# Performance work log

Measured on AMD Instinct MI355X. Metric: run time of the kernel, lower is better.

## Reference

```python
import jax, jax.numpy as jnp
import numpy as np

TIMESTEPS = 1000

def _cosine_schedule(T, s=0.008):
    # Nichol & Dhariwal cosine schedule
    x = np.linspace(0.0, T, T + 1, dtype=np.float64)
    acp = np.cos(((x / T) + s) / (1.0 + s) * np.pi / 2.0) ** 2
    acp = acp / acp[0]
    betas = np.clip(1.0 - acp[1:] / acp[:-1], 1e-4, 0.999)
    alphas_cumprod = np.cumprod(1.0 - betas)
    return (betas.astype(np.float32),
            np.sqrt(alphas_cumprod).astype(np.float32),
            np.sqrt(1.0 - alphas_cumprod).astype(np.float32))

BETAS, SQRT_ACP, SQRT_OM_ACP = _cosine_schedule(TIMESTEPS)

B = 2048            # crystals
N_PER = 64          # atoms per crystal (uniform ragged groups)
N = B * N_PER       # total atoms
NODE_DIM = 64
N_SPECIES = 100

def setup_inputs() -> dict:
    key = jax.random.key(0)
    ks = jax.random.split(key, 10)
    frac_coords = jax.random.uniform(ks[0], (N, 3), dtype=jnp.float32)
    noise = jax.random.normal(ks[1], (N, 3), dtype=jnp.float32)
    pred_noise = jax.random.normal(ks[2], (N, 3), dtype=jnp.float32)
    h_final = jax.random.normal(ks[3], (N, NODE_DIM), dtype=jnp.float32)
    # lattice: identity-dominated cells ~5 Angstrom with small perturbation
    lattice = 5.0 * jnp.eye(3, dtype=jnp.float32)[None] + 0.2 * jax.random.normal(ks[4], (B, 3, 3), dtype=jnp.float32)
    W1 = jax.random.normal(ks[5], (NODE_DIM, 128), dtype=jnp.float32) * (1.0 / np.sqrt(NODE_DIM))
    b1 = jnp.zeros((128,), dtype=jnp.float32)
    W2 = jax.random.normal(ks[6], (128, N_SPECIES), dtype=jnp.float32) * (1.0 / np.sqrt(128.0))
    b2 = jnp.zeros((N_SPECIES,), dtype=jnp.float32)
    t = jax.random.randint(ks[7], (B,), 0, TIMESTEPS)
    batch_indices = jnp.repeat(jnp.arange(B), N_PER)
    species = jax.random.randint(ks[8], (N,), 0, N_SPECIES)
    return {"frac_coords": frac_coords, "noise": noise, "pred_noise": pred_noise,
            "h_final": h_final, "lattice": lattice, "W1": W1, "b1": b1,
            "W2": W2, "b2": b2, "t": t, "batch_indices": batch_indices,
            "species": species}

def reference(frac_coords, noise, pred_noise, h_final, lattice, W1, b1, W2, b2,
              t, batch_indices, species):
    sqrt_acp = jnp.asarray(SQRT_ACP)
    sqrt_om = jnp.asarray(SQRT_OM_ACP)
    t_nodes = t[batch_indices]                       # [N]
    sa = sqrt_acp[t_nodes][:, None]                  # [N,1]
    so = sqrt_om[t_nodes][:, None]                   # [N,1]
    # q_sample + periodic wrap
    x_t = sa * frac_coords + so * noise
    x_t = x_t - jnp.floor(x_t)
    # diffusion MSE (dynamics output pred_noise supplied as input)
    loss_diffusion = jnp.mean((pred_noise - noise) ** 2)
    # predicted x0, wrapped
    pred_x0 = (x_t - so * pred_noise) / sa
    pred_x0 = pred_x0 - jnp.floor(pred_x0)
    # vectorized ragged PBC repulsion (uniform groups of N_PER atoms)
    bsz = lattice.shape[0]
    n = frac_coords.shape[0] // bsz
    f = pred_x0.reshape(bsz, n, 3)                   # [B,n,3]
    diff = f[:, :, None, :] - f[:, None, :, :]       # [B,n,n,3]
    diff = diff - jnp.round(diff)                    # minimum-image convention
    diff_c = jnp.einsum('bijk,bkl->bijl', diff, lattice)
    dist_sq = jnp.sum(diff_c ** 2, axis=-1)          # [B,n,n]
    eye = jnp.eye(n, dtype=bool)
    dist_sq = jnp.where(eye[None], 1e10, dist_sq)    # fill_diagonal_(inf)
    dist = jnp.sqrt(dist_sq + 1e-8)
    rep = jax.nn.relu(0.8 - dist) ** 2
    l_repulsion = jnp.sum(rep) / n / bsz
    loss_diffusion = loss_diffusion + 5.0 * l_repulsion
    # species head: Linear -> SiLU -> Linear, cross entropy
    hidden = jax.nn.silu(h_final @ W1 + b1)
    logits = hidden @ W2 + b2                        # [N,100]
    logp = jax.nn.log_softmax(logits, axis=-1)
    loss_species = -jnp.mean(jnp.take_along_axis(logp, species[:, None], axis=-1))
    return (loss_diffusion, loss_species, l_repulsion)
```

## Files before the change

### kernel.cpp

```cpp
#include <hip/hip_runtime.h>
#include <math.h>

#define TSTEPS   1000
#define NB       2048
#define NPER     64
#define NATOMS   (NB*NPER)
#define NDIM     64
#define NHID     128
#define NSPEC    100

typedef __attribute__((ext_vector_type(8))) short bf16x8;
typedef __attribute__((ext_vector_type(4))) float f32x4;

__device__ inline short f2bf(float x) {
  unsigned u = __builtin_bit_cast(unsigned, x);
  u += 0x7fffu + ((u >> 16) & 1u);
  return (short)(u >> 16);
}

__global__ __launch_bounds__(256) void k_sched(float* __restrict__ sacp,
                                               float* __restrict__ som,
                                               const float* __restrict__ W1,
                                               const float* __restrict__ W2,
                                               const float* __restrict__ b2,
                                               unsigned short* __restrict__ w1f,
                                               unsigned short* __restrict__ w2f,
                                               float* __restrict__ b2p) {
  const int tid = threadIdx.x, blk = blockIdx.x;
  if (blk == 0) {
    if (tid < 112) b2p[tid] = (tid < NSPEC) ? b2[tid] : 0.0f;
    __shared__ double sh[256];
    const double PI = 3.14159265358979323846, s = 0.008;
    const int t0 = tid * 4;
    double lg[4], loc = 0.0;
    if (t0 < TSTEPS) {
      double c[5];
      #pragma unroll
      for (int i = 0; i < 5; ++i) {
        double u = (((double)(t0 + i) / (double)TSTEPS) + s) / (1.0 + s) * PI * 0.5;
        c[i] = cos(u);
      }
      #pragma unroll
      for (int i = 0; i < 4; ++i) {
        double beta = 1.0 - (c[i+1]*c[i+1]) / (c[i]*c[i]);
        beta = fmin(fmax(beta, 1e-4), 0.999);
        lg[i] = log(1.0 - beta);
        loc += lg[i];
      }
    }
    sh[tid] = loc;
    __syncthreads();
    for (int off = 1; off < 256; off <<= 1) {
      double add = (tid >= off) ? sh[tid - off] : 0.0;
      __syncthreads();
      sh[tid] += add;
      __syncthreads();
    }
    if (t0 < TSTEPS) {
      double run = sh[tid] - loc;
      #pragma unroll
      for (int i = 0; i < 4; ++i) {
        run += lg[i];
        double cum = exp(run);
        sacp[t0+i] = (float)sqrt(cum);
        som[t0+i]  = (float)sqrt(1.0 - cum);
      }
    }
  } else if (blk <= 4) {
    const int c0 = (blk - 1) * 256 + tid;
    const int lane = c0 & 63, t = c0 >> 6;
    const int kk = t & 1, nt = t >> 1;
    const int q = lane >> 4, l15 = lane & 15;
    __attribute__((aligned(16))) unsigned short v[8];
    #pragma unroll
    for (int j = 0; j < 8; ++j) {
      int k = kk*32 + q*8 + j;
      v[j] = (unsigned short)f2bf(W1[k*NHID + nt*16 + l15]);
    }
    *(uint4*)(w1f + (size_t)c0*8) = *(const uint4*)v;
  } else {
    for (int c0 = (blk - 5) * 256 + tid; c0 < 3584; c0 += 1792) {
      const int lane = c0 & 63, t = c0 >> 6;
      const int kk = t & 3, nt = t >> 2;
      const int q = lane >> 4, l15 = lane & 15;
      const int cls = nt*16 + l15;
      __attribute__((aligned(16))) unsigned short v[8];
      #pragma unroll
      for (int j = 0; j < 8; ++j) {
        int k = kk*32 + q*8 + j;
        v[j] = (cls < NSPEC) ? (unsigned short)f2bf(W2[k*NSPEC + cls]) : 0;
      }
      *(uint4*)(w2f + (size_t)c0*8) = *(const uint4*)v;
    }
  }
}

__global__ __launch_bounds__(256) void k_main(const float* __restrict__ hfin,
                                              const float* __restrict__ b1,
                                              const float* __restrict__ b2p,
                                              const int*   __restrict__ spec,
                                              const unsigned short* __restrict__ w1f,
                                              const unsigned short* __restrict__ w2f,
                                              const float* __restrict__ frac,
                                              const float* __restrict__ noise,
                                              const float* __restrict__ pnoise,
                                              const float* __restrict__ lattice,
                                              const int*   __restrict__ tarr,
                                              const float* __restrict__ sacp,
                                              const float* __restrict__ som,
                                              float* __restrict__ mseP,
                                              float* __restrict__ repP,
                                              float* __restrict__ specP) {
  __shared__ __attribute__((aligned(16))) unsigned short Hs[4*2048];
  const int tid  = threadIdx.x;
  const int wave = tid >> 6, lane = tid & 63;
  const int q = lane >> 4, l15 = lane & 15;
  const int b = blockIdx.x, atomBase = b*64, slabBase = atomBase + wave*16;
  unsigned short* HsW = Hs + wave*2048;

  const int tt = tarr[b];
  const float sa = sacp[tt], so = som[tt];
  const float rsa = __builtin_amdgcn_rcpf(sa);
  float px0, px1, px2, msep;
  {
    const int a = atomBase + lane;
    const float3 fr = *(const float3*)(frac   + 3*(size_t)a);
    const float3 nz = *(const float3*)(noise  + 3*(size_t)a);
    const float3 pn = *(const float3*)(pnoise + 3*(size_t)a);
    float xt0 = fmaf(so, nz.x, sa*fr.x); xt0 -= floorf(xt0);
    float xt1 = fmaf(so, nz.y, sa*fr.y); xt1 -= floorf(xt1);
    float xt2 = fmaf(so, nz.z, sa*fr.z); xt2 -= floorf(xt2);
    px0 = (xt0 - so*pn.x)*rsa; px0 -= floorf(px0);
    px1 = (xt1 - so*pn.y)*rsa; px1 -= floorf(px1);
    px2 = (xt2 - so*pn.z)*rsa; px2 -= floorf(px2);
    float d0 = pn.x - nz.x, d1 = pn.y - nz.y, d2 = pn.z - nz.z;
    msep = fmaf(d0, d0, fmaf(d1, d1, d2*d2));
  }

  bf16x8 aF[2];
  {
    const float* rp = hfin + (size_t)(slabBase + l15) * NDIM;
    #pragma unroll
    for (int kk = 0; kk < 2; ++kk) {
      const float4 p = *(const float4*)(rp + kk*32 + q*8);
      const float4 r = *(const float4*)(rp + kk*32 + q*8 + 4);
      bf16x8 a;
      a[0]=f2bf(p.x); a[1]=f2bf(p.y); a[2]=f2bf(p.z); a[3]=f2bf(p.w);
      a[4]=f2bf(r.x); a[5]=f2bf(r.y); a[6]=f2bf(r.z); a[7]=f2bf(r.w);
      aF[kk] = a;
    }
  }

  f32x4 acc1[8];
  #pragma unroll
  for (int nt = 0; nt < 8; ++nt) acc1[nt] = (f32x4){0.f,0.f,0.f,0.f};
  #pragma unroll
  for (int nt = 0; nt < 8; ++nt) {
    #pragma unroll
    for (int kk = 0; kk < 2; ++kk) {
      bf16x8 wa = *(const bf16x8*)(w1f + (size_t)(((nt*2 + kk)*64 + lane))*8);
      acc1[nt] = __builtin_amdgcn_mfma_f32_16x16x32_bf16(wa, aF[kk], acc1[nt], 0, 0, 0);
    }
  }
  #pragma unroll
  for (int nt = 0; nt < 8; ++nt) {
    const float4 bv = *(const float4*)(b1 + nt*16 + q*4);
    float sl[4];
    #pragma unroll
    for (int r = 0; r < 4; ++r) {
      float x = acc1[nt][r] + ((const float*)&bv)[r];
      float e = __expf(-x);
      sl[r] = x * __builtin_amdgcn_rcpf(1.0f + e);
    }
    uint2 pk;
    pk.x = ((unsigned)(unsigned short)f2bf(sl[0])) | (((unsigned)(unsigned short)f2bf(sl[1])) << 16);
    pk.y = ((unsigned)(unsigned short)f2bf(sl[2])) | (((unsigned)(unsigned short)f2bf(sl[3])) << 16);
    *(uint2*)(HsW + (nt*2 + (q>>1))*128 + l15*8 + (q&1)*4) = pk;
  }
  __builtin_amdgcn_wave_barrier();

  bf16x8 a2[4];
  #pragma unroll
  for (int kk = 0; kk < 4; ++kk)
    a2[kk] = *(const bf16x8*)(HsW + (kk*4 + q)*128 + l15*8);
  f32x4 acc2[7];
  #pragma unroll
  for (int nt = 0; nt < 7; ++nt) acc2[nt] = (f32x4){0.f,0.f,0.f,0.f};
  #pragma unroll
  for (int nt = 0; nt < 7; ++nt) {
    #pragma unroll
    for (int kk = 0; kk < 4; ++kk) {
      bf16x8 wb = *(const bf16x8*)(w2f + (size_t)(((nt*4 + kk)*64 + lane))*8);
      acc2[nt] = __builtin_amdgcn_mfma_f32_16x16x32_bf16(wb, a2[kk], acc2[nt], 0, 0, 0);
    }
  }

  const int tgt = spec[slabBase + l15];
  float mx = -1e30f;
  #pragma unroll
  for (int nt = 0; nt < 7; ++nt) {
    const float4 bb = *(const float4*)(b2p + nt*16 + q*4);
    #pragma unroll
    for (int r = 0; r < 4; ++r) {
      const int cls = nt*16 + q*4 + r;
      float v = acc2[nt][r] + ((const float*)&bb)[r];
      v = (cls < NSPEC) ? v : -1e30f;
      acc2[nt][r] = v;
      mx = fmaxf(mx, v);
    }
  }
  mx = fmaxf(mx, __shfl_xor(mx, 16, 64));
  mx = fmaxf(mx, __shfl_xor(mx, 32, 64));
  float ssum = 0.0f, lt = 0.0f;
  #pragma unroll
  for (int nt = 0; nt < 7; ++nt) {
    #pragma unroll
    for (int r = 0; r < 4; ++r) {
      float v = acc2[nt][r];
      ssum += __expf(v - mx);
      lt   += (nt*16 + q*4 + r == tgt) ? v : 0.0f;
    }
  }
  ssum += __shfl_xor(ssum, 16, 64);  ssum += __shfl_xor(ssum, 32, 64);
  lt   += __shfl_xor(lt,   16, 64);  lt   += __shfl_xor(lt,   32, 64);
  float logp = lt - mx - __logf(ssum);
  #pragma unroll
  for (int d = 1; d < 16; d <<= 1) logp += __shfl_xor(logp, d, 64);

  const float* L = lattice + b*9;
  const float L00=L[0],L01=L[1],L02=L[2],
              L10=L[3],L11=L[4],L12=L[5],
              L20=L[6],L21=L[7],L22=L[8];
  float rep = 0.0f;
  #pragma unroll
  for (int it = 0; it < 16; ++it) {
    const int i = wave*16 + it;
    float xi = __shfl(px0, i, 64);
    float yi = __shfl(px1, i, 64);
    float zi = __shfl(px2, i, 64);
    if (i != lane) {
      float dx = xi - px0; dx -= rintf(dx);
      float dy = yi - px1; dy -= rintf(dy);
      float dz = zi - px2; dz -= rintf(dz);
      float cx = dx*L00 + dy*L10 + dz*L20;
      float cy = dx*L01 + dy*L11 + dz*L21;
      float cz = dx*L02 + dy*L12 + dz*L22;
      float d2 = fmaf(cx, cx, fmaf(cy, cy, cz*cz)) + 1e-8f;
      float r  = 0.8f - __builtin_amdgcn_sqrtf(d2);
      if (r > 0.0f) rep = fmaf(r, r, rep);
    }
  }
  #pragma unroll
  for (int o = 32; o > 0; o >>= 1) {
    rep  += __shfl_down(rep,  o, 64);
    msep += __shfl_down(msep, o, 64);
  }
  if (lane == 0) {
    specP[b*4 + wave] = logp;
    repP [b*4 + wave] = rep;
    if (wave == 0) mseP[b] = msep;
  }
}

__global__ __launch_bounds__(1024) void k_fin(const float* __restrict__ mseP,
                                              const float* __restrict__ repP,
                                              const float* __restrict__ specP,
                                              float* __restrict__ out) {
  __shared__ double sh[48];
  const int tid = threadIdx.x;
  double m = 0.0, r = 0.0, s = 0.0;
  for (int i = tid; i < NB*4; i += 1024) {
    r += (double)repP[i];
    s += (double)specP[i];
    if (i < NB) m += (double)mseP[i];
  }
  #pragma unroll
  for (int o = 32; o > 0; o >>= 1) {
    m += __shfl_down(m, o, 64);
    r += __shfl_down(r, o, 64);
    s += __shfl_down(s, o, 64);
  }
  const int w = tid >> 6, lane = tid & 63;
  if (lane == 0) { sh[w] = m; sh[16+w] = r; sh[32+w] = s; }
  __syncthreads();
  if (tid == 0) {
    double M=0, R=0, S=0;
    for (int i = 0; i < 16; ++i) { M += sh[i]; R += sh[16+i]; S += sh[32+i]; }
    double mse   = M / (double)(NATOMS*3);
    double lrep  = R / (double)NATOMS;
    double lspec = -S / (double)NATOMS;
    out[0] = (float)(mse + 5.0*lrep);
    out[1] = (float)lspec;
    out[2] = (float)lrep;
  }
}

extern "C" void kernel_launch(void* const* d_in, const int* in_sizes, int n_in,
                              void* d_out, int out_size, void* d_ws, size_t ws_size,
                              hipStream_t stream) {
  const float* frac    = (const float*)d_in[0];
  const float* noise   = (const float*)d_in[1];
  const float* pnoise  = (const float*)d_in[2];
  const float* hfin    = (const float*)d_in[3];
  const float* lattice = (const float*)d_in[4];
  const float* W1      = (const float*)d_in[5];
  const float* b1      = (const float*)d_in[6];
  const float* W2      = (const float*)d_in[7];
  const float* b2      = (const float*)d_in[8];
  const int*   tarr    = (const int*)d_in[9];
  const int*   spec    = (const int*)d_in[11];
  float* out = (float*)d_out;

  float*  sacp = (float*)d_ws;
  float*  som  = sacp + 1024;
  unsigned short* w1f = (unsigned short*)((char*)d_ws + 8192);
  unsigned short* w2f = (unsigned short*)((char*)d_ws + 24576);
  float* b2p   = (float*)((char*)d_ws + 53248);
  float* mseP  = (float*)((char*)d_ws + 53760);
  float* repP  = (float*)((char*)d_ws + 61952);
  float* specP = (float*)((char*)d_ws + 94720);

  k_sched<<<dim3(12), dim3(256),  0, stream>>>(sacp, som, W1, W2, b2, w1f, w2f, b2p);
  k_main <<<dim3(NB), dim3(256),  0, stream>>>(hfin, b1, b2p, spec, w1f, w2f,
                                               frac, noise, pnoise, lattice,
                                               tarr, sacp, som, mseP, repP, specP);
  k_fin  <<<dim3(1),  dim3(1024), 0, stream>>>(mseP, repP, specP, out);
}
```

Measured before the change: 128.4 us.

## Process two crystals per block and fuse final reduction via last-block atomic

Each block now handles 128 atoms (two crystals), with each wave processing two 16-atom MFMA tiles that share the same weight-fragment loads. The softmax uses an online max/sum, and the repulsion loop covers 32 rows per wave. The separate finalize kernel is removed: a global atomic counter, reset in the schedule kernel, lets the last block do the final reduction. This cuts one kernel launch and halves per-block weight loads, in exchange for more register pressure, half as many blocks, and a serialized tail reduction.

```diff
diff --git a/kernel.cpp b/kernel.cpp
--- a/kernel.cpp
+++ b/kernel.cpp
@@ -3,6 +3,7 @@
 
 #define TSTEPS   1000
 #define NB       2048
+#define NB2      1024
 #define NPER     64
 #define NATOMS   (NB*NPER)
 #define NDIM     64
@@ -25,9 +26,11 @@
                                                const float* __restrict__ b2,
                                                unsigned short* __restrict__ w1f,
                                                unsigned short* __restrict__ w2f,
-                                               float* __restrict__ b2p) {
+                                               float* __restrict__ b2p,
+                                               unsigned* __restrict__ cnt) {
   const int tid = threadIdx.x, blk = blockIdx.x;
   if (blk == 0) {
+    if (tid == 0) cnt[0] = 0u;
     if (tid < 112) b2p[tid] = (tid < NSPEC) ? b2[tid] : 0.0f;
     __shared__ double sh[256];
     const double PI = 3.14159265358979323846, s = 0.008;
@@ -110,23 +113,28 @@
                                               const float* __restrict__ som,
                                               float* __restrict__ mseP,
                                               float* __restrict__ repP,
-                                              float* __restrict__ specP) {
-  __shared__ __attribute__((aligned(16))) unsigned short Hs[4*2048];
+                                              float* __restrict__ specP,
+                                              unsigned* __restrict__ cnt,
+                                              float* __restrict__ out) {
+  __shared__ __attribute__((aligned(16))) unsigned short Hs[4*4096];
+  __shared__ int isLast;
   const int tid  = threadIdx.x;
   const int wave = tid >> 6, lane = tid & 63;
   const int q = lane >> 4, l15 = lane & 15;
-  const int b = blockIdx.x, atomBase = b*64, slabBase = atomBase + wave*16;
-  unsigned short* HsW = Hs + wave*2048;
-
-  const int tt = tarr[b];
+  const int b = blockIdx.x;
+  const int atomBase = b * 128;
+  unsigned short* HsW = Hs + wave*4096;
+
+  const int cu = __builtin_amdgcn_readfirstlane(2*b + (wave >> 1));
+  const int tt = tarr[cu];
   const float sa = sacp[tt], so = som[tt];
   const float rsa = __builtin_amdgcn_rcpf(sa);
   float px0, px1, px2, msep;
   {
-    const int a = atomBase + lane;
-    const float3 fr = *(const float3*)(frac   + 3*(size_t)a);
-    const float3 nz = *(const float3*)(noise  + 3*(size_t)a);
-    const float3 pn = *(const float3*)(pnoise + 3*(size_t)a);
+    const size_t a = (size_t)cu*64 + lane;
+    const float3 fr = *(const float3*)(frac   + 3*a);
+    const float3 nz = *(const float3*)(noise  + 3*a);
+    const float3 pn = *(const float3*)(pnoise + 3*a);
     float xt0 = fmaf(so, nz.x, sa*fr.x); xt0 -= floorf(xt0);
     float xt1 = fmaf(so, nz.y, sa*fr.y); xt1 -= floorf(xt1);
     float xt2 = fmaf(so, nz.z, sa*fr.z); xt2 -= floorf(xt2);
@@ -137,9 +145,10 @@
     msep = fmaf(d0, d0, fmaf(d1, d1, d2*d2));
   }
 
-  bf16x8 aF[2];
-  {
-    const float* rp = hfin + (size_t)(slabBase + l15) * NDIM;
+  bf16x8 aF[2][2];
+  #pragma unroll
+  for (int at = 0; at < 2; ++at) {
+    const float* rp = hfin + (size_t)(atomBase + wave*32 + at*16 + l15) * NDIM;
     #pragma unroll
     for (int kk = 0; kk < 2; ++kk) {
       const float4 p = *(const float4*)(rp + kk*32 + q*8);
@@ -147,94 +156,103 @@
       bf16x8 a;
       a[0]=f2bf(p.x); a[1]=f2bf(p.y); a[2]=f2bf(p.z); a[3]=f2bf(p.w);
       a[4]=f2bf(r.x); a[5]=f2bf(r.y); a[6]=f2bf(r.z); a[7]=f2bf(r.w);
-      aF[kk] = a;
-    }
-  }
-
-  f32x4 acc1[8];
-  #pragma unroll
-  for (int nt = 0; nt < 8; ++nt) acc1[nt] = (f32x4){0.f,0.f,0.f,0.f};
+      aF[at][kk] = a;
+    }
+  }
+
   #pragma unroll
   for (int nt = 0; nt < 8; ++nt) {
+    f32x4 dA = (f32x4){0.f,0.f,0.f,0.f}, dB = dA;
     #pragma unroll
     for (int kk = 0; kk < 2; ++kk) {
-      bf16x8 wa = *(const bf16x8*)(w1f + (size_t)(((nt*2 + kk)*64 + lane))*8);
-      acc1[nt] = __builtin_amdgcn_mfma_f32_16x16x32_bf16(wa, aF[kk], acc1[nt], 0, 0, 0);
-    }
-  }
-  #pragma unroll
-  for (int nt = 0; nt < 8; ++nt) {
+      bf16x8 wt = *(const bf16x8*)(w1f + (size_t)(((nt*2 + kk)*64 + lane))*8);
+      dA = __builtin_amdgcn_mfma_f32_16x16x32_bf16(wt, aF[0][kk], dA, 0, 0, 0);
+      dB = __builtin_amdgcn_mfma_f32_16x16x32_bf16(wt, aF[1][kk], dB, 0, 0, 0);
+    }
     const float4 bv = *(const float4*)(b1 + nt*16 + q*4);
-    float sl[4];
-    #pragma unroll
-    for (int r = 0; r < 4; ++r) {
-      float x = acc1[nt][r] + ((const float*)&bv)[r];
-      float e = __expf(-x);
-      sl[r] = x * __builtin_amdgcn_rcpf(1.0f + e);
-    }
-    uint2 pk;
-    pk.x = ((unsigned)(unsigned short)f2bf(sl[0])) | (((unsigned)(unsigned short)f2bf(sl[1])) << 16);
-    pk.y = ((unsigned)(unsigned short)f2bf(sl[2])) | (((unsigned)(unsigned short)f2bf(sl[3])) << 16);
-    *(uint2*)(HsW + (nt*2 + (q>>1))*128 + l15*8 + (q&1)*4) = pk;
+    #pragma unroll
+    for (int at = 0; at < 2; ++at) {
+      const f32x4 d = at ? dB : dA;
+      float sl[4];
+      #pragma unroll
+      for (int r = 0; r < 4; ++r) {
+        float x = d[r] + ((const float*)&bv)[r];
+        float e = __expf(-x);
+        sl[r] = x * __builtin_amdgcn_rcpf(1.0f + e);
+      }
+      uint2 pk;
+      pk.x = ((unsigned)(unsigned short)f2bf(sl[0])) | (((unsigned)(unsigned short)f2bf(sl[1])) << 16);
+      pk.y = ((unsigned)(unsigned short)f2bf(sl[2])) | (((unsigned)(unsigned short)f2bf(sl[3])) << 16);
+      *(uint2*)(HsW + at*2048 + (nt*2 + (q>>1))*128 + l15*8 + (q&1)*4) = pk;
+    }
   }
   __builtin_amdgcn_wave_barrier();
 
-  bf16x8 a2[4];
-  #pragma unroll
-  for (int kk = 0; kk < 4; ++kk)
-    a2[kk] = *(const bf16x8*)(HsW + (kk*4 + q)*128 + l15*8);
-  f32x4 acc2[7];
-  #pragma unroll
-  for (int nt = 0; nt < 7; ++nt) acc2[nt] = (f32x4){0.f,0.f,0.f,0.f};
+  bf16x8 a2[2][4];
+  #pragma unroll
+  for (int at = 0; at < 2; ++at)
+    #pragma unroll
+    for (int kk = 0; kk < 4; ++kk)
+      a2[at][kk] = *(const bf16x8*)(HsW + at*2048 + (kk*4 + q)*128 + l15*8);
+
+  const int tgtA = spec[atomBase + wave*32 + l15];
+  const int tgtB = spec[atomBase + wave*32 + 16 + l15];
+  float mA = -1e30f, sA = 0.0f, ltA = 0.0f;
+  float mB = -1e30f, sB = 0.0f, ltB = 0.0f;
   #pragma unroll
   for (int nt = 0; nt < 7; ++nt) {
+    f32x4 dA = (f32x4){0.f,0.f,0.f,0.f}, dB = dA;
     #pragma unroll
     for (int kk = 0; kk < 4; ++kk) {
-      bf16x8 wb = *(const bf16x8*)(w2f + (size_t)(((nt*4 + kk)*64 + lane))*8);
-      acc2[nt] = __builtin_amdgcn_mfma_f32_16x16x32_bf16(wb, a2[kk], acc2[nt], 0, 0, 0);
-    }
-  }
-
-  const int tgt = spec[slabBase + l15];
-  float mx = -1e30f;
-  #pragma unroll
-  for (int nt = 0; nt < 7; ++nt) {
+      bf16x8 wt = *(const bf16x8*)(w2f + (size_t)(((nt*4 + kk)*64 + lane))*8);
+      dA = __builtin_amdgcn_mfma_f32_16x16x32_bf16(wt, a2[0][kk], dA, 0, 0, 0);
+      dB = __builtin_amdgcn_mfma_f32_16x16x32_bf16(wt, a2[1][kk], dB, 0, 0, 0);
+    }
     const float4 bb = *(const float4*)(b2p + nt*16 + q*4);
+    float vA[4], vB[4], vmA = -1e30f, vmB = -1e30f;
     #pragma unroll
     for (int r = 0; r < 4; ++r) {
       const int cls = nt*16 + q*4 + r;
-      float v = acc2[nt][r] + ((const float*)&bb)[r];
-      v = (cls < NSPEC) ? v : -1e30f;
-      acc2[nt][r] = v;
-      mx = fmaxf(mx, v);
-    }
-  }
-  mx = fmaxf(mx, __shfl_xor(mx, 16, 64));
-  mx = fmaxf(mx, __shfl_xor(mx, 32, 64));
-  float ssum = 0.0f, lt = 0.0f;
-  #pragma unroll
-  for (int nt = 0; nt < 7; ++nt) {
-    #pragma unroll
-    for (int r = 0; r < 4; ++r) {
-      float v = acc2[nt][r];
-      ssum += __expf(v - mx);
-      lt   += (nt*16 + q*4 + r == tgt) ? v : 0.0f;
-    }
-  }
-  ssum += __shfl_xor(ssum, 16, 64);  ssum += __shfl_xor(ssum, 32, 64);
-  lt   += __shfl_xor(lt,   16, 64);  lt   += __shfl_xor(lt,   32, 64);
-  float logp = lt - mx - __logf(ssum);
+      float xa = dA[r] + ((const float*)&bb)[r];
+      float xb = dB[r] + ((const float*)&bb)[r];
+      xa = (cls < NSPEC) ? xa : -1e30f;
+      xb = (cls < NSPEC) ? xb : -1e30f;
+      ltA += (cls == tgtA) ? xa : 0.0f;
+      ltB += (cls == tgtB) ? xb : 0.0f;
+      vA[r] = xa; vB[r] = xb;
+      vmA = fmaxf(vmA, xa); vmB = fmaxf(vmB, xb);
+    }
+    float mnA = fmaxf(mA, vmA), mnB = fmaxf(mB, vmB);
+    sA = sA*__expf(mA - mnA) + __expf(vA[0]-mnA) + __expf(vA[1]-mnA)
+                             + __expf(vA[2]-mnA) + __expf(vA[3]-mnA);
+    sB = sB*__expf(mB - mnB) + __expf(vB[0]-mnB) + __expf(vB[1]-mnB)
+                             + __expf(vB[2]-mnB) + __expf(vB[3]-mnB);
+    mA = mnA; mB = mnB;
+  }
+  #pragma unroll
+  for (int d = 16; d <= 32; d <<= 1) {
+    float omA = __shfl_xor(mA, d, 64), osA = __shfl_xor(sA, d, 64);
+    float omB = __shfl_xor(mB, d, 64), osB = __shfl_xor(sB, d, 64);
+    float mnA = fmaxf(mA, omA), mnB = fmaxf(mB, omB);
+    sA = sA*__expf(mA - mnA) + osA*__expf(omA - mnA);
+    sB = sB*__expf(mB - mnB) + osB*__expf(omB - mnB);
+    mA = mnA; mB = mnB;
+    ltA += __shfl_xor(ltA, d, 64);
+    ltB += __shfl_xor(ltB, d, 64);
+  }
+  float logp = (ltA - mA - __logf(sA)) + (ltB - mB - __logf(sB));
   #pragma unroll
   for (int d = 1; d < 16; d <<= 1) logp += __shfl_xor(logp, d, 64);
 
-  const float* L = lattice + b*9;
+  const float* L = lattice + cu*9;
   const float L00=L[0],L01=L[1],L02=L[2],
               L10=L[3],L11=L[4],L12=L[5],
               L20=L[6],L21=L[7],L22=L[8];
+  const int ibase = (wave & 1) * 32;
   float rep = 0.0f;
-  #pragma unroll
-  for (int it = 0; it < 16; ++it) {
-    const int i = wave*16 + it;
+  #pragma unroll 8
+  for (int it = 0; it < 32; ++it) {
+    const int i = ibase + it;
     float xi = __shfl(px0, i, 64);
     float yi = __shfl(px1, i, 64);
     float zi = __shfl(px2, i, 64);
@@ -258,40 +276,43 @@
   if (lane == 0) {
     specP[b*4 + wave] = logp;
     repP [b*4 + wave] = rep;
-    if (wave == 0) mseP[b] = msep;
-  }
-}
-
-__global__ __launch_bounds__(1024) void k_fin(const float* __restrict__ mseP,
-                                              const float* __restrict__ repP,
-                                              const float* __restrict__ specP,
-                                              float* __restrict__ out) {
-  __shared__ double sh[48];
-  const int tid = threadIdx.x;
-  double m = 0.0, r = 0.0, s = 0.0;
-  for (int i = tid; i < NB*4; i += 1024) {
-    r += (double)repP[i];
-    s += (double)specP[i];
-    if (i < NB) m += (double)mseP[i];
-  }
-  #pragma unroll
-  for (int o = 32; o > 0; o >>= 1) {
-    m += __shfl_down(m, o, 64);
-    r += __shfl_down(r, o, 64);
-    s += __shfl_down(s, o, 64);
-  }
-  const int w = tid >> 6, lane = tid & 63;
-  if (lane == 0) { sh[w] = m; sh[16+w] = r; sh[32+w] = s; }
+    if ((wave & 1) == 0) mseP[b*2 + (wave>>1)] = msep;
+  }
+
+  __threadfence();
+  if (tid == 0) {
+    unsigned v = atomicAdd(cnt, 1u);
+    isLast = (v == NB2 - 1u) ? 1 : 0;
+  }
   __syncthreads();
-  if (tid == 0) {
-    double M=0, R=0, S=0;
-    for (int i = 0; i < 16; ++i) { M += sh[i]; R += sh[16+i]; S += sh[32+i]; }
-    double mse   = M / (double)(NATOMS*3);
-    double lrep  = R / (double)NATOMS;
-    double lspec = -S / (double)NATOMS;
-    out[0] = (float)(mse + 5.0*lrep);
-    out[1] = (float)lspec;
-    out[2] = (float)lrep;
+  if (isLast) {
+    __threadfence();
+    __shared__ double sh[12];
+    double m = 0.0, r = 0.0, s = 0.0;
+    for (int i = tid; i < NB2*4; i += 256) {
+      r += (double)repP[i];
+      s += (double)specP[i];
+      if (i < NB2*2) m += (double)mseP[i];
+    }
+    #pragma unroll
+    for (int o = 32; o > 0; o >>= 1) {
+      m += __shfl_down(m, o, 64);
+      r += __shfl_down(r, o, 64);
+      s += __shfl_down(s, o, 64);
+    }
+    if (lane == 0) { sh[wave] = m; sh[4+wave] = r; sh[8+wave] = s; }
+    __syncthreads();
+    if (tid == 0) {
+      double M = sh[0]+sh[1]+sh[2]+sh[3];
+      double R = sh[4]+sh[5]+sh[6]+sh[7];
+      double S = sh[8]+sh[9]+sh[10]+sh[11];
+      double mse   = M / (double)(NATOMS*3);
+      double lrep  = R / (double)NATOMS;
+      double lspec = -S / (double)NATOMS;
+      out[0] = (float)(mse + 5.0*lrep);
+      out[1] = (float)lspec;
+      out[2] = (float)lrep;
+    }
   }
 }
 
@@ -316,13 +337,14 @@
   unsigned short* w1f = (unsigned short*)((char*)d_ws + 8192);
   unsigned short* w2f = (unsigned short*)((char*)d_ws + 24576);
   float* b2p   = (float*)((char*)d_ws + 53248);
+  unsigned* cnt = (unsigned*)((char*)d_ws + 53696);
   float* mseP  = (float*)((char*)d_ws + 53760);
   float* repP  = (float*)((char*)d_ws + 61952);
-  float* specP = (float*)((char*)d_ws + 94720);
-
-  k_sched<<<dim3(12), dim3(256),  0, stream>>>(sacp, som, W1, W2, b2, w1f, w2f, b2p);
-  k_main <<<dim3(NB), dim3(256),  0, stream>>>(hfin, b1, b2p, spec, w1f, w2f,
+  float* specP = (float*)((char*)d_ws + 78336);
+
+  k_sched<<<dim3(12),  dim3(256), 0, stream>>>(sacp, som, W1, W2, b2, w1f, w2f, b2p, cnt);
+  k_main <<<dim3(NB2), dim3(256), 0, stream>>>(hfin, b1, b2p, spec, w1f, w2f,
                                                frac, noise, pnoise, lattice,
-                                               tarr, sacp, som, mseP, repP, specP);
-  k_fin  <<<dim3(1),  dim3(1024), 0, stream>>>(mseP, repP, specP, out);
+                                               tarr, sacp, som, mseP, repP, specP,
+                                               cnt, out);
 }
```

After: 194.8 us. 1.52x slower.
